# Kernel tuning notes

Hardware: AMD Instinct MI355X
Metric: run time of the kernel (lower is better)

The kernel has to match this reference:

```python
import jax, jax.numpy as jnp
import numpy as np

B, H, N, C, E, D, L_OUT, LAYERS = 16, 64, 512, 3, 128, 32, 12, 2


def setup_inputs() -> dict:
    key = jax.random.key(0)
    ks = jax.random.split(key, 16)
    nrm = lambda k, s, sc=1.0: jax.random.normal(k, s, jnp.float32) * sc
    adj = jax.random.uniform(ks[0], (N, N), jnp.float32)
    adj = adj / adj.sum(axis=-1, keepdims=True)  # row-normalized prior adjacency
    return {
        "x_input": nrm(ks[1], (B, H, N, C)),
        "adj": adj,
        "Wf": nrm(ks[2], (3, E, 3 * C), 0.1),
        "Uf": nrm(ks[3], (3, E, E), 0.05),
        "bf": jnp.zeros((3, E), jnp.float32),
        "E1f": nrm(ks[4], (N, D)),
        "E2f": nrm(ks[5], (N, D)),
        "Wb": nrm(ks[6], (3, E, 3 * C), 0.1),
        "Ub": nrm(ks[7], (3, E, E), 0.05),
        "bb": jnp.zeros((3, E), jnp.float32),
        "E1b": nrm(ks[8], (N, D)),
        "E2b": nrm(ks[9], (N, D)),
        "dec_w": nrm(ks[10], (L_OUT, LAYERS, 2 * E), 0.05),  # Conv2d(layer_num->out_len, k=(1,2E)) squeezed
        "dec_b": jnp.zeros((L_OUT,), jnp.float32),
        "out_w": nrm(ks[11], (L_OUT, L_OUT), 0.1),  # 1x1 Conv2d squeezed
        "out_b": jnp.zeros((L_OUT,), jnp.float32),
    }


def _cell_step(c, xt, adj, A_dyn, W, U, b):
    # Graph-coupled GRU cell (IBNCell): xt [B,C,N], c [B,E,N].
    msg = jnp.concatenate(
        [xt,
         jnp.einsum('bcn,nm->bcm', xt, adj),      # prior-graph message passing
         jnp.einsum('bcn,nm->bcm', xt, A_dyn)],   # learned dynamic-graph message passing
        axis=1)  # [B, 3C, N]
    gx = jnp.einsum('goc,bcn->gbon', W, msg)  # 3 stacked gate projections
    r = jax.nn.sigmoid(gx[0] + jnp.einsum('oe,ben->bon', U[0], c) + b[0][:, None])
    u = jax.nn.sigmoid(gx[1] + jnp.einsum('oe,ben->bon', U[1], c) + b[1][:, None])
    g = jnp.tanh(gx[2] + jnp.einsum('oe,ben->bon', U[2], r * c) + b[2][:, None])
    return u * c + (1.0 - u) * g


def _forward(x_input, adj, Wf, Uf, bf, E1f, E2f, Wb, Ub, bb, E1b, E2b, dec_w, dec_b, out_w, out_b):
    # torch: x_input.transpose(-3,-1).transpose(-2,-1) -> [B,C,H,N]; scan layout [H,B,C,N]
    xs = jnp.transpose(x_input, (1, 0, 3, 2))
    A_f = jax.nn.softmax(jax.nn.relu(E1f @ E2f.T), axis=-1)  # dynamic adjacency, fwd cell
    A_b = jax.nn.softmax(jax.nn.relu(E1b @ E2b.T), axis=-1)  # dynamic adjacency, back cell
    c0 = jnp.zeros((xs.shape[1], Wf.shape[1], xs.shape[3]), xs.dtype)  # [B,E,N]

    def step_f(c, xt):
        cn = _cell_step(c, xt, adj, A_f, Wf, Uf, bf)
        return cn, None

    # Output only depends on the last timestep of the bidirectional concat:
    # forward branch -> final state after H steps; backward branch (after flip)
    # at t=H-1 -> its FIRST step (input x[H-1]). Dead per-step outputs elided.
    h_fwd, _ = jax.lax.scan(step_f, c0, xs)
    h_back0 = _cell_step(c0, xs[-1], adj, A_b, Wb, Ub, bb)
    last_ht = jnp.concatenate([h_fwd, h_back0], axis=1)  # [B, 2E, N]

    lt = jnp.transpose(last_ht, (0, 2, 1))  # [B, N, 2E]
    # layer loop z>0 is a no-op on current_layer_output -> final_result repeats last_ht
    final = jnp.broadcast_to(lt[:, None], (lt.shape[0], LAYERS, lt.shape[1], lt.shape[2]))
    h = jnp.einsum('blne,ole->bon', final, dec_w) + dec_b[:, None]  # decoder conv (1,2E)
    return jnp.einsum('oi,bin->bon', out_w, h) + out_b[:, None]  # 1x1 output conv -> [B,L_OUT,N]


def reference(x_input, adj, Wf, Uf, bf, E1f, E2f, Wb, Ub, bb, E1b, E2b, dec_w, dec_b, out_w, out_b):
    return _forward(x_input, adj, Wf, Uf, bf, E1f, E2f, Wb, Ub, bb, E1b, E2b, dec_w, dec_b, out_w, out_b)
```

## Files before the change

kernel.cpp:

```cpp
#include <hip/hip_runtime.h>


typedef _Float16 half8_t __attribute__((ext_vector_type(8)));
typedef float float4_t __attribute__((ext_vector_type(4)));

#define PIN(x) asm volatile("" : "+v"(x))

__device__ __forceinline__ float sigmoidf_(float x) {
  return __builtin_amdgcn_rcpf(1.f + __expf(-x));
}
__device__ __forceinline__ float tanhf_(float x) {
  return fmaf(-2.f, __builtin_amdgcn_rcpf(__expf(2.f * x) + 1.f), 1.f);
}

__global__ __launch_bounds__(256) void prep_kernel(
    const float* __restrict__ E1f, const float* __restrict__ E2f,
    const float* __restrict__ E1b, const float* __restrict__ E2b,
    const float* __restrict__ adj, const float* __restrict__ x,
    const float* __restrict__ Wf, const float* __restrict__ Uf,
    const float* __restrict__ bf, const float* __restrict__ Wb,
    const float* __restrict__ bb, _Float16* __restrict__ adjT,
    _Float16* __restrict__ AfT, _Float16* __restrict__ AbT,
    _Float16* __restrict__ xT16, _Float16* __restrict__ ufrag,
    _Float16* __restrict__ wbfrag) {
  int bid = blockIdx.x;
  int tid = threadIdx.x;
  if (bid >= 1288) {
    int bid2 = bid - 1288;
    int b = bid2 >> 6, t = bid2 & 63;
    const float2* xp = (const float2*)(x + (size_t)(b * 64 + t) * 1536);
    float2 f0 = xp[tid * 3], f1 = xp[tid * 3 + 1], f2 = xp[tid * 3 + 2];
    _Float16* dst = xT16 + (size_t)(b * 64 + t) * 1536;
    int n0_ = tid * 2;
    dst[n0_] = (_Float16)f0.x;
    dst[512 + n0_] = (_Float16)f0.y;
    dst[1024 + n0_] = (_Float16)f1.x;
    dst[n0_ + 1] = (_Float16)f1.y;
    dst[512 + n0_ + 1] = (_Float16)f2.x;
    dst[1024 + n0_ + 1] = (_Float16)f2.y;
    return;
  }
  if (bid >= 1272) {
    int r2 = bid - 1272;
    int gi = 1 + (r2 & 1);
    int og = r2 >> 1;
    for (int e = tid; e < 512; e += 256) {
      int lane = e >> 3, j = e & 7;
      int o = og * 16 + (lane & 15);
      int q = (lane >> 4) * 8 + j;
      float v = (q < 9) ? Wb[gi * 1152 + o * 9 + q]
                        : (q == 9 ? bb[gi * 128 + o] : 0.f);
      wbfrag[r2 * 512 + e] = (_Float16)v;
    }
    return;
  }
  if (bid >= 1152) {
    int r = bid - 1152;
    int kb = r % 5;
    int gi = (r / 5) % 3;
    int og = r / 15;
    for (int e = tid; e < 512; e += 256) {
      int lane = e >> 3, j = e & 7;
      int o = og * 16 + (lane & 15);
      int q4 = lane >> 4;
      float v;
      if (kb < 4) {
        v = Uf[gi * 16384 + o * 128 + kb * 32 + q4 * 8 + j];
      } else {
        int q = q4 * 8 + j;
        v = (q < 9) ? Wf[gi * 1152 + o * 9 + q]
                    : (q == 9 ? bf[gi * 128 + o] : 0.f);
      }
      ufrag[r * 512 + e] = (_Float16)v;
    }
    return;
  }
  if (bid >= 1024) {
    int base = (bid - 1024) * 4;
    for (int r = 0; r < 4; ++r) {
      int row = base + r;
      float v0 = adj[row * 512 + tid];
      float v1 = adj[row * 512 + tid + 256];
      adjT[(size_t)tid * 512 + row] = (_Float16)v0;
      adjT[(size_t)(tid + 256) * 512 + row] = (_Float16)v1;
    }
    return;
  }
  int which = bid >> 9;
  int row = bid & 511;
  const float* E1 = which ? E1b : E1f;
  const float* E2 = which ? E2b : E2f;
  _Float16* A = which ? AbT : AfT;
  __shared__ float e1s[32];
  __shared__ float red[256];
  if (tid < 32) e1s[tid] = E1[row * 32 + tid];
  __syncthreads();
  float s[2];
#pragma unroll
  for (int h = 0; h < 2; ++h) {
    int m = tid + h * 256;
    const float4* e2 = (const float4*)(E2 + m * 32);
    float acc = 0.f;
#pragma unroll
    for (int d4 = 0; d4 < 8; ++d4) {
      float4 v = e2[d4];
      acc = fmaf(v.x, e1s[d4 * 4 + 0], acc);
      acc = fmaf(v.y, e1s[d4 * 4 + 1], acc);
      acc = fmaf(v.z, e1s[d4 * 4 + 2], acc);
      acc = fmaf(v.w, e1s[d4 * 4 + 3], acc);
    }
    s[h] = fmaxf(acc, 0.f);
  }
  red[tid] = fmaxf(s[0], s[1]);
  __syncthreads();
  for (int off = 128; off > 0; off >>= 1) {
    if (tid < off) red[tid] = fmaxf(red[tid], red[tid + off]);
    __syncthreads();
  }
  float mx = red[0];
  __syncthreads();
  float e0 = __expf(s[0] - mx), e1v = __expf(s[1] - mx);
  red[tid] = e0 + e1v;
  __syncthreads();
  for (int off = 128; off > 0; off >>= 1) {
    if (tid < off) red[tid] += red[tid + off];
    __syncthreads();
  }
  float inv = __builtin_amdgcn_rcpf(red[0]);
  A[(size_t)tid * 512 + row] = (_Float16)(e0 * inv);
  A[(size_t)(tid + 256) * 512 + row] = (_Float16)(e1v * inv);
}

__global__ __launch_bounds__(256, 4) void msg_kernel(
    const _Float16* __restrict__ xT16, const _Float16* __restrict__ adjT,
    const _Float16* __restrict__ AfT, const _Float16* __restrict__ AbT,
    _Float16* __restrict__ msg16, _Float16* __restrict__ msgb16) {
  __shared__ __align__(8) _Float16 Sst[512 * 12];
  int tid = threadIdx.x;
  int t = blockIdx.x >> 4;
  int n0g = (blockIdx.x & 15) * 32;
  int lane = tid & 63, og = tid >> 6;
  int l15 = lane & 15, q4 = lane >> 4, q0 = q4 * 8;
  int nt = og & 1, mat = og >> 1;
  bool is63 = (t == 63);
  bool doAb = is63 && (mat == 0);

  const _Float16* Bmat = mat ? AfT : adjT;
  int n = n0g + nt * 16 + l15;

  const float4_t zero4 = {0.f, 0.f, 0.f, 0.f};
  float4_t acc[3], accb[3];
#pragma unroll
  for (int mt = 0; mt < 3; ++mt) { acc[mt] = zero4; accb[mt] = zero4; }

  for (int kb = 0; kb < 16; ++kb) {
    half8_t b0 = *(const half8_t*)&Bmat[(size_t)n * 512 + kb * 32 + q0];
    half8_t b2;
    if (doAb) b2 = *(const half8_t*)&AbT[(size_t)n * 512 + kb * 32 + q0];
#pragma unroll
    for (int mt = 0; mt < 3; ++mt) {
      int m = mt * 16 + l15;
      int bm = (m * 21846) >> 16;
      int cm = m - bm * 3;
      half8_t a = *(const half8_t*)
          &xT16[((size_t)(bm * 64 + t) * 3 + cm) * 512 + kb * 32 + q0];
      acc[mt] = __builtin_amdgcn_mfma_f32_16x16x32_f16(a, b0, acc[mt], 0, 0, 0);
      if (doAb)
        accb[mt] = __builtin_amdgcn_mfma_f32_16x16x32_f16(a, b2, accb[mt], 0, 0, 0);
    }
  }

  for (int i = tid; i < 512; i += 256) {
    int tb = i >> 5, nl = i & 31;
    int nn = n0g + nl;
    _Float16* row = &Sst[i * 12];
#pragma unroll
    for (int c = 0; c < 3; ++c)
      row[c] = xT16[((size_t)(tb * 64 + t) * 3 + c) * 512 + nn];
    row[9] = (_Float16)1.f;
    row[10] = (_Float16)0.f;
    row[11] = (_Float16)0.f;
  }
#pragma unroll
  for (int mt = 0; mt < 3; ++mt)
#pragma unroll
    for (int r = 0; r < 4; ++r) {
      int m = mt * 16 + q4 * 4 + r;
      int tb = (m * 21846) >> 16;
      int c = m - tb * 3;
      Sst[((size_t)tb * 32 + nt * 16 + l15) * 12 + 3 + mat * 3 + c] =
          (_Float16)acc[mt][r];
    }
  __syncthreads();
  for (int i = tid; i < 512; i += 256) {
    int tb = i >> 5, nl = i & 31;
    const uint2* s = (const uint2*)&Sst[i * 12];
    uint2* dst = (uint2*)&msg16[((size_t)(t * 16 + tb) * 512 + n0g + nl) * 12];
    dst[0] = s[0]; dst[1] = s[1]; dst[2] = s[2];
  }
  if (is63) {
    __syncthreads();
    if (mat == 0) {
#pragma unroll
      for (int mt = 0; mt < 3; ++mt)
#pragma unroll
        for (int r = 0; r < 4; ++r) {
          int m = mt * 16 + q4 * 4 + r;
          int tb = (m * 21846) >> 16;
          int c = m - tb * 3;
          Sst[((size_t)tb * 32 + nt * 16 + l15) * 12 + 6 + c] = (_Float16)accb[mt][r];
        }
    }
    __syncthreads();
    for (int i = tid; i < 512; i += 256) {
      int tb = i >> 5, nl = i & 31;
      const uint2* s = (const uint2*)&Sst[i * 12];
      uint2* dst = (uint2*)&msgb16[((size_t)tb * 512 + n0g + nl) * 12];
      dst[0] = s[0]; dst[1] = s[1]; dst[2] = s[2];
    }
  }
}

__global__ __launch_bounds__(512, 4) void rec_kernel(
    const _Float16* __restrict__ msg16, const _Float16* __restrict__ msgb16,
    const _Float16* __restrict__ ufrag, const _Float16* __restrict__ wbfrag,
    const float* __restrict__ dec_w, const float* __restrict__ dec_b,
    const float* __restrict__ out_w, const float* __restrict__ out_b,
    float* __restrict__ out) {
  __shared__ __align__(16) _Float16 Cbuf[4 * 64 * 8];
  __shared__ __align__(16) _Float16 Gbuf[4 * 64 * 8];
  __shared__ float hf_lds[128 * 16];
  __shared__ float hb_lds[128 * 16];
  __shared__ float hdec_lds[12 * 16];
  int tid = threadIdx.x, bid = blockIdx.x;
  int b = bid >> 5;
  int n0 = (bid & 31) * 16;
  int lane = tid & 63, og = tid >> 6;
  int l15 = lane & 15, q4 = lane >> 4;

  half8_t afrag[3][5];
#pragma unroll
  for (int gi = 0; gi < 3; ++gi)
#pragma unroll
    for (int kb = 0; kb < 5; ++kb) {
      afrag[gi][kb] = *(const half8_t*)
          &ufrag[(size_t)(((og * 3 + gi) * 5 + kb) * 512) + lane * 8];
      PIN(afrag[gi][kb]);
    }

  if (tid < 256) {
    uint4 z; z.x = z.y = z.z = z.w = 0;
    ((uint4*)Cbuf)[tid] = z;
  }
  float cr[4] = {0.f, 0.f, 0.f, 0.f};
  __syncthreads();

  const float4_t zero4 = {0.f, 0.f, 0.f, 0.f};
  union H4U { _Float16 h[4]; unsigned long long u; };
  union U16 { uint4 u4; half8_t h8; };
  unsigned odd = q4 & 1;
  const char* mrow = (const char*)msg16 + ((size_t)(b * 512 + n0 + l15)) * 24;
  const size_t tstride = (size_t)16 * 512 * 24;

  U16 bu;
  {
    uint4 lo = *(const uint4*)mrow;
    uint2 hi = *(const uint2*)(mrow + 16);
    bu.u4.x = odd ? hi.x : lo.x;
    bu.u4.y = odd ? hi.y : lo.y;
    bu.u4.z = odd ? 0u : lo.z;
    bu.u4.w = odd ? 0u : lo.w;
  }
  half8_t bm_cur = bu.h8;

  int kb_w = og >> 1;
  int lane_w = ((og & 1) * 2 + (q4 >> 1)) * 16 + l15;
  int j0 = (q4 & 1) * 4;

  for (int t = 0; t < 64; ++t) {
    int tn = (t < 63) ? t + 1 : 63;
    const char* p = mrow + (size_t)tn * tstride;
    uint4 lo = *(const uint4*)p;
    uint2 hi = *(const uint2*)(p + 16);

    half8_t cf[4];
#pragma unroll
    for (int kb = 0; kb < 4; ++kb)
      cf[kb] = *(const half8_t*)&Cbuf[(kb * 64 + lane) * 8];

    float4_t accr = zero4, accu = zero4;
#pragma unroll
    for (int kb = 0; kb < 4; ++kb) {
      accr = __builtin_amdgcn_mfma_f32_16x16x32_f16(afrag[0][kb], cf[kb], accr, 0, 0, 0);
      accu = __builtin_amdgcn_mfma_f32_16x16x32_f16(afrag[1][kb], cf[kb], accu, 0, 0, 0);
    }
    accr = __builtin_amdgcn_mfma_f32_16x16x32_f16(afrag[0][4], bm_cur, accr, 0, 0, 0);
    accu = __builtin_amdgcn_mfma_f32_16x16x32_f16(afrag[1][4], bm_cur, accu, 0, 0, 0);
    float4_t accg = __builtin_amdgcn_mfma_f32_16x16x32_f16(afrag[2][4], bm_cur, zero4, 0, 0, 0);

    {
      H4U v;
#pragma unroll
      for (int r = 0; r < 4; ++r)
        v.h[r] = (_Float16)(sigmoidf_(accr[r]) * cr[r]);
      *(unsigned long long*)&Gbuf[(kb_w * 64 + lane_w) * 8 + j0] = v.u;
    }
    __syncthreads();

    half8_t gf[4];
#pragma unroll
    for (int kb = 0; kb < 4; ++kb)
      gf[kb] = *(const half8_t*)&Gbuf[(kb * 64 + lane) * 8];
#pragma unroll
    for (int kb = 0; kb < 4; ++kb)
      accg = __builtin_amdgcn_mfma_f32_16x16x32_f16(afrag[2][kb], gf[kb], accg, 0, 0, 0);

    {
      H4U v;
#pragma unroll
      for (int r = 0; r < 4; ++r) {
        float uu = sigmoidf_(accu[r]);
        float gg = tanhf_(accg[r]);
        float cn = fmaf(uu, cr[r] - gg, gg);
        cr[r] = cn;
        v.h[r] = (_Float16)cn;
      }
      *(unsigned long long*)&Cbuf[(kb_w * 64 + lane_w) * 8 + j0] = v.u;
    }
    __syncthreads();

    bu.u4.x = odd ? hi.x : lo.x;
    bu.u4.y = odd ? hi.y : lo.y;
    bu.u4.z = odd ? 0u : lo.z;
    bu.u4.w = odd ? 0u : lo.w;
    bm_cur = bu.h8;
  }

  {
    const char* p = (const char*)msgb16 + ((size_t)(b * 512 + n0 + l15)) * 24;
    uint4 lo = *(const uint4*)p;
    uint2 hi = *(const uint2*)(p + 16);
    U16 bb2;
    bb2.u4.x = odd ? hi.x : lo.x;
    bb2.u4.y = odd ? hi.y : lo.y;
    bb2.u4.z = odd ? 0u : lo.z;
    bb2.u4.w = odd ? 0u : lo.w;
    half8_t au_f = *(const half8_t*)&wbfrag[(size_t)((og * 2 + 0) * 512) + lane * 8];
    half8_t ag_f = *(const half8_t*)&wbfrag[(size_t)((og * 2 + 1) * 512) + lane * 8];
    float4_t au = __builtin_amdgcn_mfma_f32_16x16x32_f16(au_f, bb2.h8, zero4, 0, 0, 0);
    float4_t ag = __builtin_amdgcn_mfma_f32_16x16x32_f16(ag_f, bb2.h8, zero4, 0, 0, 0);
#pragma unroll
    for (int r = 0; r < 4; ++r) {
      int row = og * 16 + q4 * 4 + r;
      float uu = sigmoidf_(au[r]);
      float gg = tanhf_(ag[r]);
      hb_lds[row * 16 + l15] = (1.f - uu) * gg;
      hf_lds[row * 16 + l15] = cr[r];
    }
  }
  __syncthreads();

  if (tid < 192) {
    int i = tid >> 4, cc = tid & 15;
    const float* dwa = dec_w + (size_t)i * 512;
    const float* dwb = dwa + 256;
    float hd = dec_b[i];
    for (int e = 0; e < 128; ++e) {
      hd = fmaf(dwa[e] + dwb[e], hf_lds[e * 16 + cc], hd);
      hd = fmaf(dwa[128 + e] + dwb[128 + e], hb_lds[e * 16 + cc], hd);
    }
    hdec_lds[i * 16 + cc] = hd;
  }
  __syncthreads();
  if (tid < 192) {
    int o = tid >> 4, cc = tid & 15;
    float v = out_b[o];
#pragma unroll
    for (int i = 0; i < 12; ++i) v = fmaf(out_w[o * 12 + i], hdec_lds[i * 16 + cc], v);
    out[((size_t)(b * 12 + o)) * 512 + n0 + cc] = v;
  }
}

extern "C" void kernel_launch(void* const* d_in, const int* in_sizes, int n_in,
                              void* d_out, int out_size, void* d_ws, size_t ws_size,
                              hipStream_t stream) {
  (void)in_sizes; (void)n_in; (void)out_size; (void)ws_size;
  const float* x     = (const float*)d_in[0];
  const float* adj   = (const float*)d_in[1];
  const float* Wf    = (const float*)d_in[2];
  const float* Uf    = (const float*)d_in[3];
  const float* bf    = (const float*)d_in[4];
  const float* E1f   = (const float*)d_in[5];
  const float* E2f   = (const float*)d_in[6];
  const float* Wb    = (const float*)d_in[7];
  const float* bb    = (const float*)d_in[9];
  const float* E1b   = (const float*)d_in[10];
  const float* E2b   = (const float*)d_in[11];
  const float* dec_w = (const float*)d_in[12];
  const float* dec_b = (const float*)d_in[13];
  const float* out_w = (const float*)d_in[14];
  const float* out_b = (const float*)d_in[15];

  _Float16* h      = (_Float16*)d_ws;
  _Float16* adjT   = h;
  _Float16* AfT    = h + 262144;
  _Float16* AbT    = h + 524288;
  _Float16* xT16   = h + 786432;
  _Float16* ufrag  = h + 2359296;
  _Float16* wbfrag = h + 2420736;
  _Float16* msg16  = h + 2428928;
  _Float16* msgb16 = h + 8720384;

  prep_kernel<<<2312, 256, 0, stream>>>(E1f, E2f, E1b, E2b, adj, x, Wf, Uf, bf,
                                        Wb, bb, adjT, AfT, AbT, xT16, ufrag, wbfrag);
  msg_kernel<<<1024, 256, 0, stream>>>(xT16, adjT, AfT, AbT, msg16, msgb16);
  rec_kernel<<<512, 512, 0, stream>>>(msg16, msgb16, ufrag, wbfrag,
                                      dec_w, dec_b, out_w, out_b, (float*)d_out);
}
```

Baseline: 220.0 us.

## Interleave two node groups per block in GRU recurrence to hide barrier latency

Each recurrence block now processes two 16-node groups (32 nodes) instead of one, halving the grid to 256 blocks. The two groups' phases are interleaved so one group's reset-gate matmul overlaps the other's candidate-gate matmul, cutting barriers per timestep roughly in half relative to the work done. Prefetching of the next timestep's message is spread across the phases. The cost is fewer blocks (256 on a GPU with many CUs), more registers per thread and lower occupancy via the launch bound change.

Result: slower. 235.0 us (+6.8%).

```diff
diff --git a/kernel.cpp b/kernel.cpp
--- a/kernel.cpp
+++ b/kernel.cpp
@@ -221,20 +221,20 @@
   }
 }
 
-__global__ __launch_bounds__(512, 4) void rec_kernel(
+__global__ __launch_bounds__(512, 2) void rec_kernel(
     const _Float16* __restrict__ msg16, const _Float16* __restrict__ msgb16,
     const _Float16* __restrict__ ufrag, const _Float16* __restrict__ wbfrag,
     const float* __restrict__ dec_w, const float* __restrict__ dec_b,
     const float* __restrict__ out_w, const float* __restrict__ out_b,
     float* __restrict__ out) {
-  __shared__ __align__(16) _Float16 Cbuf[4 * 64 * 8];
-  __shared__ __align__(16) _Float16 Gbuf[4 * 64 * 8];
-  __shared__ float hf_lds[128 * 16];
-  __shared__ float hb_lds[128 * 16];
-  __shared__ float hdec_lds[12 * 16];
+  __shared__ __align__(16) _Float16 Cbuf[2][2048];
+  __shared__ __align__(16) _Float16 Gbuf[2][2048];
+  __shared__ float hf_lds[128 * 32];
+  __shared__ float hb_lds[128 * 32];
+  __shared__ float hdec_lds[12 * 32];
   int tid = threadIdx.x, bid = blockIdx.x;
-  int b = bid >> 5;
-  int n0 = (bid & 31) * 16;
+  int b = bid >> 4;
+  int n0 = (bid & 15) * 32;
   int lane = tid & 63, og = tid >> 6;
   int l15 = lane & 15, q4 = lane >> 4;
 
@@ -248,135 +248,148 @@
       PIN(afrag[gi][kb]);
     }
 
-  if (tid < 256) {
+  {
     uint4 z; z.x = z.y = z.z = z.w = 0;
-    ((uint4*)Cbuf)[tid] = z;
-  }
-  float cr[4] = {0.f, 0.f, 0.f, 0.f};
-  __syncthreads();
+    ((uint4*)&Cbuf[0][0])[tid] = z;
+  }
 
   const float4_t zero4 = {0.f, 0.f, 0.f, 0.f};
   union H4U { _Float16 h[4]; unsigned long long u; };
   union U16 { uint4 u4; half8_t h8; };
   unsigned odd = q4 & 1;
-  const char* mrow = (const char*)msg16 + ((size_t)(b * 512 + n0 + l15)) * 24;
   const size_t tstride = (size_t)16 * 512 * 24;
-
-  U16 bu;
-  {
-    uint4 lo = *(const uint4*)mrow;
-    uint2 hi = *(const uint2*)(mrow + 16);
-    bu.u4.x = odd ? hi.x : lo.x;
-    bu.u4.y = odd ? hi.y : lo.y;
-    bu.u4.z = odd ? 0u : lo.z;
-    bu.u4.w = odd ? 0u : lo.w;
-  }
-  half8_t bm_cur = bu.h8;
+  const char* mrow[2];
+  mrow[0] = (const char*)msg16 + ((size_t)(b * 512 + n0 + l15)) * 24;
+  mrow[1] = mrow[0] + 16 * 24;
+
+  float cr[2][4] = {{0.f, 0.f, 0.f, 0.f}, {0.f, 0.f, 0.f, 0.f}};
+  float4_t accu[2], accg[2];
+  uint4 pf_lo[2];
+  uint2 pf_hi[2];
+#pragma unroll
+  for (int g = 0; g < 2; ++g) {
+    pf_lo[g] = *(const uint4*)mrow[g];
+    pf_hi[g] = *(const uint2*)(mrow[g] + 16);
+  }
 
   int kb_w = og >> 1;
   int lane_w = ((og & 1) * 2 + (q4 >> 1)) * 16 + l15;
   int j0 = (q4 & 1) * 4;
 
-  for (int t = 0; t < 64; ++t) {
-    int tn = (t < 63) ? t + 1 : 63;
-    const char* p = mrow + (size_t)tn * tstride;
-    uint4 lo = *(const uint4*)p;
-    uint2 hi = *(const uint2*)(p + 16);
-
+  auto P1 = [&](int g, int tn) {
+    U16 bu;
+    bu.u4.x = odd ? pf_hi[g].x : pf_lo[g].x;
+    bu.u4.y = odd ? pf_hi[g].y : pf_lo[g].y;
+    bu.u4.z = odd ? 0u : pf_lo[g].z;
+    bu.u4.w = odd ? 0u : pf_lo[g].w;
+    half8_t bm = bu.h8;
     half8_t cf[4];
 #pragma unroll
     for (int kb = 0; kb < 4; ++kb)
-      cf[kb] = *(const half8_t*)&Cbuf[(kb * 64 + lane) * 8];
-
-    float4_t accr = zero4, accu = zero4;
+      cf[kb] = *(const half8_t*)&Cbuf[g][(kb * 64 + lane) * 8];
+    float4_t accr = zero4;
+    float4_t au = zero4;
 #pragma unroll
     for (int kb = 0; kb < 4; ++kb) {
       accr = __builtin_amdgcn_mfma_f32_16x16x32_f16(afrag[0][kb], cf[kb], accr, 0, 0, 0);
-      accu = __builtin_amdgcn_mfma_f32_16x16x32_f16(afrag[1][kb], cf[kb], accu, 0, 0, 0);
-    }
-    accr = __builtin_amdgcn_mfma_f32_16x16x32_f16(afrag[0][4], bm_cur, accr, 0, 0, 0);
-    accu = __builtin_amdgcn_mfma_f32_16x16x32_f16(afrag[1][4], bm_cur, accu, 0, 0, 0);
-    float4_t accg = __builtin_amdgcn_mfma_f32_16x16x32_f16(afrag[2][4], bm_cur, zero4, 0, 0, 0);
-
-    {
-      H4U v;
-#pragma unroll
-      for (int r = 0; r < 4; ++r)
-        v.h[r] = (_Float16)(sigmoidf_(accr[r]) * cr[r]);
-      *(unsigned long long*)&Gbuf[(kb_w * 64 + lane_w) * 8 + j0] = v.u;
-    }
-    __syncthreads();
-
+      au = __builtin_amdgcn_mfma_f32_16x16x32_f16(afrag[1][kb], cf[kb], au, 0, 0, 0);
+    }
+    accr = __builtin_amdgcn_mfma_f32_16x16x32_f16(afrag[0][4], bm, accr, 0, 0, 0);
+    accu[g] = __builtin_amdgcn_mfma_f32_16x16x32_f16(afrag[1][4], bm, au, 0, 0, 0);
+    accg[g] = __builtin_amdgcn_mfma_f32_16x16x32_f16(afrag[2][4], bm, zero4, 0, 0, 0);
+    const char* p = mrow[g] + (size_t)tn * tstride;
+    pf_lo[g] = *(const uint4*)p;
+    pf_hi[g] = *(const uint2*)(p + 16);
+    H4U v;
+#pragma unroll
+    for (int r = 0; r < 4; ++r)
+      v.h[r] = (_Float16)(sigmoidf_(accr[r]) * cr[g][r]);
+    *(unsigned long long*)&Gbuf[g][(kb_w * 64 + lane_w) * 8 + j0] = v.u;
+  };
+
+  auto P2 = [&](int g) {
     half8_t gf[4];
 #pragma unroll
     for (int kb = 0; kb < 4; ++kb)
-      gf[kb] = *(const half8_t*)&Gbuf[(kb * 64 + lane) * 8];
+      gf[kb] = *(const half8_t*)&Gbuf[g][(kb * 64 + lane) * 8];
+    float4_t ag = accg[g];
 #pragma unroll
     for (int kb = 0; kb < 4; ++kb)
-      accg = __builtin_amdgcn_mfma_f32_16x16x32_f16(afrag[2][kb], gf[kb], accg, 0, 0, 0);
-
-    {
-      H4U v;
-#pragma unroll
-      for (int r = 0; r < 4; ++r) {
-        float uu = sigmoidf_(accu[r]);
-        float gg = tanhf_(accg[r]);
-        float cn = fmaf(uu, cr[r] - gg, gg);
-        cr[r] = cn;
-        v.h[r] = (_Float16)cn;
-      }
-      *(unsigned long long*)&Cbuf[(kb_w * 64 + lane_w) * 8 + j0] = v.u;
-    }
-    __syncthreads();
-
-    bu.u4.x = odd ? hi.x : lo.x;
-    bu.u4.y = odd ? hi.y : lo.y;
-    bu.u4.z = odd ? 0u : lo.z;
-    bu.u4.w = odd ? 0u : lo.w;
-    bm_cur = bu.h8;
-  }
+      ag = __builtin_amdgcn_mfma_f32_16x16x32_f16(afrag[2][kb], gf[kb], ag, 0, 0, 0);
+    H4U v;
+#pragma unroll
+    for (int r = 0; r < 4; ++r) {
+      float uu = sigmoidf_(accu[g][r]);
+      float gg = tanhf_(ag[r]);
+      float cn = fmaf(uu, cr[g][r] - gg, gg);
+      cr[g][r] = cn;
+      v.h[r] = (_Float16)cn;
+    }
+    *(unsigned long long*)&Cbuf[g][(kb_w * 64 + lane_w) * 8 + j0] = v.u;
+  };
+
+  __syncthreads();
+  P1(0, 1);
+  __syncthreads();
+  for (int t = 0; t < 63; ++t) {
+    P1(1, t + 1);
+    P2(0);
+    __syncthreads();
+    int tn2 = (t < 61) ? t + 2 : 63;
+    P1(0, tn2);
+    P2(1);
+    __syncthreads();
+  }
+  P1(1, 63);
+  P2(0);
+  __syncthreads();
+  P2(1);
 
   {
-    const char* p = (const char*)msgb16 + ((size_t)(b * 512 + n0 + l15)) * 24;
-    uint4 lo = *(const uint4*)p;
-    uint2 hi = *(const uint2*)(p + 16);
-    U16 bb2;
-    bb2.u4.x = odd ? hi.x : lo.x;
-    bb2.u4.y = odd ? hi.y : lo.y;
-    bb2.u4.z = odd ? 0u : lo.z;
-    bb2.u4.w = odd ? 0u : lo.w;
     half8_t au_f = *(const half8_t*)&wbfrag[(size_t)((og * 2 + 0) * 512) + lane * 8];
     half8_t ag_f = *(const half8_t*)&wbfrag[(size_t)((og * 2 + 1) * 512) + lane * 8];
-    float4_t au = __builtin_amdgcn_mfma_f32_16x16x32_f16(au_f, bb2.h8, zero4, 0, 0, 0);
-    float4_t ag = __builtin_amdgcn_mfma_f32_16x16x32_f16(ag_f, bb2.h8, zero4, 0, 0, 0);
-#pragma unroll
-    for (int r = 0; r < 4; ++r) {
-      int row = og * 16 + q4 * 4 + r;
-      float uu = sigmoidf_(au[r]);
-      float gg = tanhf_(ag[r]);
-      hb_lds[row * 16 + l15] = (1.f - uu) * gg;
-      hf_lds[row * 16 + l15] = cr[r];
-    }
-  }
-  __syncthreads();
-
-  if (tid < 192) {
-    int i = tid >> 4, cc = tid & 15;
+#pragma unroll
+    for (int g = 0; g < 2; ++g) {
+      const char* p = (const char*)msgb16 +
+                      ((size_t)(b * 512 + n0 + g * 16 + l15)) * 24;
+      uint4 lo = *(const uint4*)p;
+      uint2 hi = *(const uint2*)(p + 16);
+      U16 bu;
+      bu.u4.x = odd ? hi.x : lo.x;
+      bu.u4.y = odd ? hi.y : lo.y;
+      bu.u4.z = odd ? 0u : lo.z;
+      bu.u4.w = odd ? 0u : lo.w;
+      float4_t au = __builtin_amdgcn_mfma_f32_16x16x32_f16(au_f, bu.h8, zero4, 0, 0, 0);
+      float4_t ag = __builtin_amdgcn_mfma_f32_16x16x32_f16(ag_f, bu.h8, zero4, 0, 0, 0);
+#pragma unroll
+      for (int r = 0; r < 4; ++r) {
+        int row = og * 16 + q4 * 4 + r;
+        float uu = sigmoidf_(au[r]);
+        float gg = tanhf_(ag[r]);
+        hb_lds[row * 32 + g * 16 + l15] = (1.f - uu) * gg;
+        hf_lds[row * 32 + g * 16 + l15] = cr[g][r];
+      }
+    }
+  }
+  __syncthreads();
+
+  if (tid < 384) {
+    int i = tid >> 5, cc = tid & 31;
     const float* dwa = dec_w + (size_t)i * 512;
     const float* dwb = dwa + 256;
     float hd = dec_b[i];
     for (int e = 0; e < 128; ++e) {
-      hd = fmaf(dwa[e] + dwb[e], hf_lds[e * 16 + cc], hd);
-      hd = fmaf(dwa[128 + e] + dwb[128 + e], hb_lds[e * 16 + cc], hd);
-    }
-    hdec_lds[i * 16 + cc] = hd;
-  }
-  __syncthreads();
-  if (tid < 192) {
-    int o = tid >> 4, cc = tid & 15;
+      hd = fmaf(dwa[e] + dwb[e], hf_lds[e * 32 + cc], hd);
+      hd = fmaf(dwa[128 + e] + dwb[128 + e], hb_lds[e * 32 + cc], hd);
+    }
+    hdec_lds[i * 32 + cc] = hd;
+  }
+  __syncthreads();
+  if (tid < 384) {
+    int o = tid >> 5, cc = tid & 31;
     float v = out_b[o];
 #pragma unroll
-    for (int i = 0; i < 12; ++i) v = fmaf(out_w[o * 12 + i], hdec_lds[i * 16 + cc], v);
+    for (int i = 0; i < 12; ++i) v = fmaf(out_w[o * 12 + i], hdec_lds[i * 32 + cc], v);
     out[((size_t)(b * 12 + o)) * 512 + n0 + cc] = v;
   }
 }
@@ -414,6 +427,6 @@
   prep_kernel<<<2312, 256, 0, stream>>>(E1f, E2f, E1b, E2b, adj, x, Wf, Uf, bf,
                                         Wb, bb, adjT, AfT, AbT, xT16, ufrag, wbfrag);
   msg_kernel<<<1024, 256, 0, stream>>>(xT16, adjT, AfT, AbT, msg16, msgb16);
-  rec_kernel<<<512, 512, 0, stream>>>(msg16, msgb16, ufrag, wbfrag,
+  rec_kernel<<<256, 512, 0, stream>>>(msg16, msgb16, ufrag, wbfrag,
                                       dec_w, dec_b, out_w, out_b, (float*)d_out);
 }
```

## Fuse message-passing GEMM into recurrent kernel and prescale gate weights for exp2

Applied to the files above, without the earlier changes.

Removes the separate msg_kernel launch. Each recurrent block now computes its own prior and dynamic graph messages for all 64 timesteps of its (batch, node-tile) with MFMA, then writes them to a block-private contiguous scratch region that is read back with a small fixed stride. Gate weights are prescaled by -log2(e) or 2·log2(e) during prep, so sigmoid and tanh reduce to a raw exp2 plus rcp, and fp16 packing uses cvt_pkrtz. In exchange each rec block does extra GEMM work up front and round-trips its messages through global memory, and the round-toward-zero conversion slightly changes numerics.

New measurement: 211.0 us. -4.1%, faster.

```diff
diff --git a/kernel.cpp b/kernel.cpp
--- a/kernel.cpp
+++ b/kernel.cpp
@@ -2,16 +2,13 @@
 
 
 typedef _Float16 half8_t __attribute__((ext_vector_type(8)));
+typedef __fp16 fp16x2_t __attribute__((ext_vector_type(2)));
 typedef float float4_t __attribute__((ext_vector_type(4)));
 
 #define PIN(x) asm volatile("" : "+v"(x))
 
-__device__ __forceinline__ float sigmoidf_(float x) {
-  return __builtin_amdgcn_rcpf(1.f + __expf(-x));
-}
-__device__ __forceinline__ float tanhf_(float x) {
-  return fmaf(-2.f, __builtin_amdgcn_rcpf(__expf(2.f * x) + 1.f), 1.f);
-}
+__device__ __forceinline__ float exp2_(float x) { return __builtin_amdgcn_exp2f(x); }
+__device__ __forceinline__ float rcp_(float x) { return __builtin_amdgcn_rcpf(x); }
 
 __global__ __launch_bounds__(256) void prep_kernel(
     const float* __restrict__ E1f, const float* __restrict__ E2f,
@@ -21,8 +18,8 @@
     const float* __restrict__ bf, const float* __restrict__ Wb,
     const float* __restrict__ bb, _Float16* __restrict__ adjT,
     _Float16* __restrict__ AfT, _Float16* __restrict__ AbT,
-    _Float16* __restrict__ xT16, _Float16* __restrict__ ufrag,
-    _Float16* __restrict__ wbfrag) {
+    _Float16* __restrict__ ufrag, _Float16* __restrict__ wbfrag,
+    _Float16* __restrict__ xT16) {
   int bid = blockIdx.x;
   int tid = threadIdx.x;
   if (bid >= 1288) {
@@ -44,13 +41,14 @@
     int r2 = bid - 1272;
     int gi = 1 + (r2 & 1);
     int og = r2 >> 1;
+    float scl = (gi == 2) ? 2.8853902f : -1.4426950f;
     for (int e = tid; e < 512; e += 256) {
       int lane = e >> 3, j = e & 7;
       int o = og * 16 + (lane & 15);
       int q = (lane >> 4) * 8 + j;
       float v = (q < 9) ? Wb[gi * 1152 + o * 9 + q]
                         : (q == 9 ? bb[gi * 128 + o] : 0.f);
-      wbfrag[r2 * 512 + e] = (_Float16)v;
+      wbfrag[r2 * 512 + e] = (_Float16)(v * scl);
     }
     return;
   }
@@ -59,6 +57,7 @@
     int kb = r % 5;
     int gi = (r / 5) % 3;
     int og = r / 15;
+    float scl = (gi == 2) ? 2.8853902f : -1.4426950f;
     for (int e = tid; e < 512; e += 256) {
       int lane = e >> 3, j = e & 7;
       int o = og * 16 + (lane & 15);
@@ -71,7 +70,7 @@
         v = (q < 9) ? Wf[gi * 1152 + o * 9 + q]
                     : (q == 9 ? bf[gi * 128 + o] : 0.f);
       }
-      ufrag[r * 512 + e] = (_Float16)v;
+      ufrag[r * 512 + e] = (_Float16)(v * scl);
     }
     return;
   }
@@ -126,117 +125,101 @@
     if (tid < off) red[tid] += red[tid + off];
     __syncthreads();
   }
-  float inv = __builtin_amdgcn_rcpf(red[0]);
+  float inv = rcp_(red[0]);
   A[(size_t)tid * 512 + row] = (_Float16)(e0 * inv);
   A[(size_t)(tid + 256) * 512 + row] = (_Float16)(e1v * inv);
 }
 
-__global__ __launch_bounds__(256, 4) void msg_kernel(
+__global__ __launch_bounds__(512, 4) void rec_kernel(
     const _Float16* __restrict__ xT16, const _Float16* __restrict__ adjT,
     const _Float16* __restrict__ AfT, const _Float16* __restrict__ AbT,
-    _Float16* __restrict__ msg16, _Float16* __restrict__ msgb16) {
-  __shared__ __align__(8) _Float16 Sst[512 * 12];
-  int tid = threadIdx.x;
-  int t = blockIdx.x >> 4;
-  int n0g = (blockIdx.x & 15) * 32;
-  int lane = tid & 63, og = tid >> 6;
-  int l15 = lane & 15, q4 = lane >> 4, q0 = q4 * 8;
-  int nt = og & 1, mat = og >> 1;
-  bool is63 = (t == 63);
-  bool doAb = is63 && (mat == 0);
-
-  const _Float16* Bmat = mat ? AfT : adjT;
-  int n = n0g + nt * 16 + l15;
-
-  const float4_t zero4 = {0.f, 0.f, 0.f, 0.f};
-  float4_t acc[3], accb[3];
-#pragma unroll
-  for (int mt = 0; mt < 3; ++mt) { acc[mt] = zero4; accb[mt] = zero4; }
-
-  for (int kb = 0; kb < 16; ++kb) {
-    half8_t b0 = *(const half8_t*)&Bmat[(size_t)n * 512 + kb * 32 + q0];
-    half8_t b2;
-    if (doAb) b2 = *(const half8_t*)&AbT[(size_t)n * 512 + kb * 32 + q0];
-#pragma unroll
-    for (int mt = 0; mt < 3; ++mt) {
-      int m = mt * 16 + l15;
-      int bm = (m * 21846) >> 16;
-      int cm = m - bm * 3;
-      half8_t a = *(const half8_t*)
-          &xT16[((size_t)(bm * 64 + t) * 3 + cm) * 512 + kb * 32 + q0];
-      acc[mt] = __builtin_amdgcn_mfma_f32_16x16x32_f16(a, b0, acc[mt], 0, 0, 0);
-      if (doAb)
-        accb[mt] = __builtin_amdgcn_mfma_f32_16x16x32_f16(a, b2, accb[mt], 0, 0, 0);
-    }
-  }
-
-  for (int i = tid; i < 512; i += 256) {
-    int tb = i >> 5, nl = i & 31;
-    int nn = n0g + nl;
-    _Float16* row = &Sst[i * 12];
-#pragma unroll
-    for (int c = 0; c < 3; ++c)
-      row[c] = xT16[((size_t)(tb * 64 + t) * 3 + c) * 512 + nn];
-    row[9] = (_Float16)1.f;
-    row[10] = (_Float16)0.f;
-    row[11] = (_Float16)0.f;
-  }
-#pragma unroll
-  for (int mt = 0; mt < 3; ++mt)
-#pragma unroll
-    for (int r = 0; r < 4; ++r) {
-      int m = mt * 16 + q4 * 4 + r;
-      int tb = (m * 21846) >> 16;
-      int c = m - tb * 3;
-      Sst[((size_t)tb * 32 + nt * 16 + l15) * 12 + 3 + mat * 3 + c] =
-          (_Float16)acc[mt][r];
-    }
-  __syncthreads();
-  for (int i = tid; i < 512; i += 256) {
-    int tb = i >> 5, nl = i & 31;
-    const uint2* s = (const uint2*)&Sst[i * 12];
-    uint2* dst = (uint2*)&msg16[((size_t)(t * 16 + tb) * 512 + n0g + nl) * 12];
-    dst[0] = s[0]; dst[1] = s[1]; dst[2] = s[2];
-  }
-  if (is63) {
-    __syncthreads();
-    if (mat == 0) {
-#pragma unroll
-      for (int mt = 0; mt < 3; ++mt)
-#pragma unroll
-        for (int r = 0; r < 4; ++r) {
-          int m = mt * 16 + q4 * 4 + r;
-          int tb = (m * 21846) >> 16;
-          int c = m - tb * 3;
-          Sst[((size_t)tb * 32 + nt * 16 + l15) * 12 + 6 + c] = (_Float16)accb[mt][r];
-        }
-    }
-    __syncthreads();
-    for (int i = tid; i < 512; i += 256) {
-      int tb = i >> 5, nl = i & 31;
-      const uint2* s = (const uint2*)&Sst[i * 12];
-      uint2* dst = (uint2*)&msgb16[((size_t)tb * 512 + n0g + nl) * 12];
-      dst[0] = s[0]; dst[1] = s[1]; dst[2] = s[2];
-    }
-  }
-}
-
-__global__ __launch_bounds__(512, 4) void rec_kernel(
-    const _Float16* __restrict__ msg16, const _Float16* __restrict__ msgb16,
+    _Float16* __restrict__ msgS, _Float16* __restrict__ msgbS,
     const _Float16* __restrict__ ufrag, const _Float16* __restrict__ wbfrag,
     const float* __restrict__ dec_w, const float* __restrict__ dec_b,
     const float* __restrict__ out_w, const float* __restrict__ out_b,
     float* __restrict__ out) {
-  __shared__ __align__(16) _Float16 Cbuf[4 * 64 * 8];
-  __shared__ __align__(16) _Float16 Gbuf[4 * 64 * 8];
+  __shared__ __align__(16) _Float16 Sst[1024 * 12];
+  __shared__ __align__(16) _Float16 Sb[64];
+  __shared__ __align__(16) _Float16 Cbuf[2048];
+  __shared__ __align__(16) _Float16 Gbuf[2048];
   __shared__ float hf_lds[128 * 16];
   __shared__ float hb_lds[128 * 16];
   __shared__ float hdec_lds[12 * 16];
   int tid = threadIdx.x, bid = blockIdx.x;
   int b = bid >> 5;
-  int n0 = (bid & 31) * 16;
+  int nt = bid & 31;
+  int n0 = nt * 16;
+  size_t s = (size_t)bid;
   int lane = tid & 63, og = tid >> 6;
-  int l15 = lane & 15, q4 = lane >> 4;
+  int l15 = lane & 15, q4 = lane >> 4, q0 = q4 * 8;
+  const float4_t zero4 = {0.f, 0.f, 0.f, 0.f};
+
+  {
+    int chunk = og >> 1, mat = og & 1;
+    const _Float16* Bmat = mat ? AfT : adjT;
+    int n = n0 + l15;
+    float4_t acc[3];
+    acc[0] = zero4; acc[1] = zero4; acc[2] = zero4;
+    float4_t accb = zero4;
+    for (int kb = 0; kb < 16; ++kb) {
+      half8_t bfrg = *(const half8_t*)&Bmat[(size_t)n * 512 + kb * 32 + q0];
+#pragma unroll
+      for (int mt = 0; mt < 3; ++mt) {
+        int m = mt * 16 + l15;
+        int tl = (m * 21846) >> 16;
+        int c = m - tl * 3;
+        int t = chunk * 16 + tl;
+        half8_t a = *(const half8_t*)
+            &xT16[((size_t)(b * 64 + t) * 3 + c) * 512 + kb * 32 + q0];
+        acc[mt] = __builtin_amdgcn_mfma_f32_16x16x32_f16(a, bfrg, acc[mt], 0, 0, 0);
+      }
+      if (og == 7) {
+        half8_t b2 = *(const half8_t*)&AbT[(size_t)n * 512 + kb * 32 + q0];
+        int c = l15 % 3;
+        half8_t a = *(const half8_t*)
+            &xT16[((size_t)(b * 64 + 63) * 3 + c) * 512 + kb * 32 + q0];
+        accb = __builtin_amdgcn_mfma_f32_16x16x32_f16(a, b2, accb, 0, 0, 0);
+      }
+    }
+    for (int i = tid; i < 1024; i += 512) {
+      int t = i >> 4, nl = i & 15;
+      _Float16* row = &Sst[i * 12];
+#pragma unroll
+      for (int c = 0; c < 3; ++c)
+        row[c] = xT16[((size_t)(b * 64 + t) * 3 + c) * 512 + n0 + nl];
+      row[9] = (_Float16)1.f;
+      row[10] = (_Float16)0.f;
+      row[11] = (_Float16)0.f;
+    }
+#pragma unroll
+    for (int mt = 0; mt < 3; ++mt)
+#pragma unroll
+      for (int r = 0; r < 4; ++r) {
+        int m = mt * 16 + q4 * 4 + r;
+        int tl = (m * 21846) >> 16;
+        int c = m - tl * 3;
+        int t = chunk * 16 + tl;
+        Sst[(t * 16 + l15) * 12 + 3 + mat * 3 + c] = (_Float16)acc[mt][r];
+      }
+    if (og == 7 && q4 == 0) {
+#pragma unroll
+      for (int r = 0; r < 3; ++r) Sb[l15 * 4 + r] = (_Float16)accb[r];
+    }
+  }
+  __syncthreads();
+  {
+    uint2* dst = (uint2*)msgS + s * 3072;
+    const uint2* src = (const uint2*)Sst;
+    for (int i = tid; i < 3072; i += 512) dst[i] = src[i];
+  }
+  if (tid < 16) {
+    int nl = tid;
+    _Float16* d = msgbS + s * 192 + nl * 12;
+#pragma unroll
+    for (int j = 0; j < 12; ++j)
+      d[j] = (j >= 6 && j < 9) ? Sb[nl * 4 + (j - 6)]
+                               : Sst[(63 * 16 + nl) * 12 + j];
+  }
 
   half8_t afrag[3][5];
 #pragma unroll
@@ -247,20 +230,22 @@
           &ufrag[(size_t)(((og * 3 + gi) * 5 + kb) * 512) + lane * 8];
       PIN(afrag[gi][kb]);
     }
-
   if (tid < 256) {
     uint4 z; z.x = z.y = z.z = z.w = 0;
     ((uint4*)Cbuf)[tid] = z;
   }
   float cr[4] = {0.f, 0.f, 0.f, 0.f};
-  __syncthreads();
-
-  const float4_t zero4 = {0.f, 0.f, 0.f, 0.f};
-  union H4U { _Float16 h[4]; unsigned long long u; };
+
+  union H4U { fp16x2_t h2[2]; unsigned long long u; };
   union U16 { uint4 u4; half8_t h8; };
   unsigned odd = q4 & 1;
-  const char* mrow = (const char*)msg16 + ((size_t)(b * 512 + n0 + l15)) * 24;
-  const size_t tstride = (size_t)16 * 512 * 24;
+  const char* mrow = (const char*)msgS + s * 24576 + l15 * 24;
+  const size_t tstride = 384;
+
+  int kb_w = og >> 1;
+  int lane_w = ((og & 1) * 2 + (q4 >> 1)) * 16 + l15;
+  int j0 = (q4 & 1) * 4;
+  __syncthreads();
 
   U16 bu;
   {
@@ -271,11 +256,7 @@
     bu.u4.z = odd ? 0u : lo.z;
     bu.u4.w = odd ? 0u : lo.w;
   }
-  half8_t bm_cur = bu.h8;
-
-  int kb_w = og >> 1;
-  int lane_w = ((og & 1) * 2 + (q4 >> 1)) * 16 + l15;
-  int j0 = (q4 & 1) * 4;
+  half8_t bm = bu.h8;
 
   for (int t = 0; t < 64; ++t) {
     int tn = (t < 63) ? t + 1 : 63;
@@ -294,16 +275,22 @@
       accr = __builtin_amdgcn_mfma_f32_16x16x32_f16(afrag[0][kb], cf[kb], accr, 0, 0, 0);
       accu = __builtin_amdgcn_mfma_f32_16x16x32_f16(afrag[1][kb], cf[kb], accu, 0, 0, 0);
     }
-    accr = __builtin_amdgcn_mfma_f32_16x16x32_f16(afrag[0][4], bm_cur, accr, 0, 0, 0);
-    accu = __builtin_amdgcn_mfma_f32_16x16x32_f16(afrag[1][4], bm_cur, accu, 0, 0, 0);
-    float4_t accg = __builtin_amdgcn_mfma_f32_16x16x32_f16(afrag[2][4], bm_cur, zero4, 0, 0, 0);
-
+    accr = __builtin_amdgcn_mfma_f32_16x16x32_f16(afrag[0][4], bm, accr, 0, 0, 0);
+    accu = __builtin_amdgcn_mfma_f32_16x16x32_f16(afrag[1][4], bm, accu, 0, 0, 0);
+    float4_t accg_p = __builtin_amdgcn_mfma_f32_16x16x32_f16(afrag[2][4], bm, zero4, 0, 0, 0);
+
+    float uu[4];
     {
       H4U v;
 #pragma unroll
-      for (int r = 0; r < 4; ++r)
-        v.h[r] = (_Float16)(sigmoidf_(accr[r]) * cr[r]);
+      for (int r = 0; r < 2; ++r) {
+        float a = rcp_(1.f + exp2_(accr[2 * r])) * cr[2 * r];
+        float bq = rcp_(1.f + exp2_(accr[2 * r + 1])) * cr[2 * r + 1];
+        v.h2[r] = __builtin_amdgcn_cvt_pkrtz(a, bq);
+      }
       *(unsigned long long*)&Gbuf[(kb_w * 64 + lane_w) * 8 + j0] = v.u;
+#pragma unroll
+      for (int r = 0; r < 4; ++r) uu[r] = rcp_(1.f + exp2_(accu[r]));
     }
     __syncthreads();
 
@@ -311,20 +298,22 @@
 #pragma unroll
     for (int kb = 0; kb < 4; ++kb)
       gf[kb] = *(const half8_t*)&Gbuf[(kb * 64 + lane) * 8];
+    float4_t accg = accg_p;
 #pragma unroll
     for (int kb = 0; kb < 4; ++kb)
       accg = __builtin_amdgcn_mfma_f32_16x16x32_f16(afrag[2][kb], gf[kb], accg, 0, 0, 0);
 
     {
       H4U v;
+      float cn[4];
 #pragma unroll
       for (int r = 0; r < 4; ++r) {
-        float uu = sigmoidf_(accu[r]);
-        float gg = tanhf_(accg[r]);
-        float cn = fmaf(uu, cr[r] - gg, gg);
-        cr[r] = cn;
-        v.h[r] = (_Float16)cn;
-      }
+        float gg = fmaf(-2.f, rcp_(exp2_(accg[r]) + 1.f), 1.f);
+        cn[r] = fmaf(uu[r], cr[r] - gg, gg);
+        cr[r] = cn[r];
+      }
+      v.h2[0] = __builtin_amdgcn_cvt_pkrtz(cn[0], cn[1]);
+      v.h2[1] = __builtin_amdgcn_cvt_pkrtz(cn[2], cn[3]);
       *(unsigned long long*)&Cbuf[(kb_w * 64 + lane_w) * 8 + j0] = v.u;
     }
     __syncthreads();
@@ -333,13 +322,13 @@
     bu.u4.y = odd ? hi.y : lo.y;
     bu.u4.z = odd ? 0u : lo.z;
     bu.u4.w = odd ? 0u : lo.w;
-    bm_cur = bu.h8;
+    bm = bu.h8;
   }
 
   {
-    const char* p = (const char*)msgb16 + ((size_t)(b * 512 + n0 + l15)) * 24;
-    uint4 lo = *(const uint4*)p;
-    uint2 hi = *(const uint2*)(p + 16);
+    const char* bp = (const char*)msgbS + s * 384 + l15 * 24;
+    uint4 lo = *(const uint4*)bp;
+    uint2 hi = *(const uint2*)(bp + 16);
     U16 bb2;
     bb2.u4.x = odd ? hi.x : lo.x;
     bb2.u4.y = odd ? hi.y : lo.y;
@@ -352,9 +341,9 @@
 #pragma unroll
     for (int r = 0; r < 4; ++r) {
       int row = og * 16 + q4 * 4 + r;
-      float uu = sigmoidf_(au[r]);
-      float gg = tanhf_(ag[r]);
-      hb_lds[row * 16 + l15] = (1.f - uu) * gg;
+      float uu2 = rcp_(1.f + exp2_(au[r]));
+      float gg = fmaf(-2.f, rcp_(exp2_(ag[r]) + 1.f), 1.f);
+      hb_lds[row * 16 + l15] = (1.f - uu2) * gg;
       hf_lds[row * 16 + l15] = cr[r];
     }
   }
@@ -405,15 +394,15 @@
   _Float16* adjT   = h;
   _Float16* AfT    = h + 262144;
   _Float16* AbT    = h + 524288;
-  _Float16* xT16   = h + 786432;
-  _Float16* ufrag  = h + 2359296;
-  _Float16* wbfrag = h + 2420736;
-  _Float16* msg16  = h + 2428928;
-  _Float16* msgb16 = h + 8720384;
+  _Float16* ufrag  = h + 786432;
+  _Float16* wbfrag = h + 847872;
+  _Float16* xT16   = h + 856064;
+  _Float16* msgS   = h + 2428928;
+  _Float16* msgbS  = h + 8720384;
 
   prep_kernel<<<2312, 256, 0, stream>>>(E1f, E2f, E1b, E2b, adj, x, Wf, Uf, bf,
-                                        Wb, bb, adjT, AfT, AbT, xT16, ufrag, wbfrag);
-  msg_kernel<<<1024, 256, 0, stream>>>(xT16, adjT, AfT, AbT, msg16, msgb16);
-  rec_kernel<<<512, 512, 0, stream>>>(msg16, msgb16, ufrag, wbfrag,
-                                      dec_w, dec_b, out_w, out_b, (float*)d_out);
+                                        Wb, bb, adjT, AfT, AbT, ufrag, wbfrag, xT16);
+  rec_kernel<<<512, 512, 0, stream>>>(xT16, adjT, AfT, AbT, msgS, msgbS,
+                                      ufrag, wbfrag, dec_w, dec_b, out_w, out_b,
+                                      (float*)d_out);
 }
```
